# Optimization experiments

Measured on AMD Instinct MI355X. Metric: run time of the kernel, lower is better.

The kernel has to match this reference:

```python
import jax, jax.numpy as jnp
import numpy as np

LN_EPS = 1e-5

def _layer_norm(x, gamma, beta):
    mu = x.mean(-1, keepdims=True)
    var = ((x - mu) ** 2).mean(-1, keepdims=True)
    return (x - mu) * jax.lax.rsqrt(var + LN_EPS) * gamma + beta

def _neg_sq_dist(q, p):
    # q: [B,Qtot,H], p: [B,N,H] -> [B,Qtot,N]
    return -jnp.sum((q[:, :, None, :] - p[:, None, :, :]) ** 2, axis=-1)

def setup_inputs() -> dict:
    key = jax.random.key(0)
    k1, k2 = jax.random.split(key)
    B, N, K, Q, H = 512, 10, 5, 5, 256
    Qtot = N * Q  # na_rate = 0
    return {
        "support": jax.random.normal(k1, (B, N * K, H), dtype=jnp.float32),
        "query": jax.random.normal(k2, (B, Qtot, H), dtype=jnp.float32),
        "ln_gamma": jnp.ones((H,), dtype=jnp.float32),
        "ln_beta": jnp.zeros((H,), dtype=jnp.float32),
        "N": N,
        "K": K,
        "Q": Q,
    }

def reference(support, query, ln_gamma, ln_beta, N, K, Q):
    B, _, H = support.shape
    s = _layer_norm(support, ln_gamma, ln_beta).reshape(B, N, K, H)
    q = _layer_norm(query, ln_gamma, ln_beta)          # [B, Qtot, H]
    Qtot = q.shape[1]

    M = s.mean(axis=2)                                  # [B, N, H] mean prototype
    # --- __rectify__ ---
    Xq = _neg_sq_dist(q, M)                             # [B, Qtot, N]
    Cq = jnp.argmax(Xq, axis=-1)                        # [B, Qtot] nearest proto
    # padded support memory [B, N, K+Qtot, H]
    Xp = jnp.pad(s, ((0, 0), (0, 0), (0, Qtot), (0, 0)))
    b_idx = jnp.arange(B)[:, None]
    q_idx = jnp.arange(Qtot)[None, :]
    # each (b,q) writes a unique slot q+K -> no collisions
    Xp = Xp.at[b_idx, Cq, q_idx + K].set(q)
    counts = jax.nn.one_hot(Cq, N, dtype=jnp.float32).sum(axis=1)  # [B, N]
    Xp_size = (K + counts)[:, :, None]                  # [B, N, 1]

    scores = jnp.einsum("bnsh,bnh->bns", Xp, M)[..., None]  # [B,N,S,1]
    M_cos = jax.nn.softmax(scores, axis=1)              # softmax over N dim
    proto = (M_cos * Xp).sum(axis=-2) / Xp_size          # [B, N, H]
    # --- logits ---
    logits = _neg_sq_dist(q, proto)                     # [B, Qtot, N]
    minn = logits.min(axis=-1, keepdims=True)
    logits = jnp.concatenate([logits, minn - 1.0], axis=-1)  # [B, Qtot, N+1]
    pred = jnp.argmax(logits.reshape(-1, N + 1), axis=1)
    return logits, pred
```

## Files before the change

kernel.cpp:

```cpp
#include <hip/hip_runtime.h>
#include <math.h>

#define LN_EPS 1e-5f

constexpr int Nn  = 10;
constexpr int Kk  = 5;
constexpr int Hh  = 256;
constexpr int QT  = 50;
constexpr int NP1 = 11;

template<int CTRL, int RM>
__device__ __forceinline__ float dpp_term(float x) {
    return __int_as_float(__builtin_amdgcn_update_dpp(
        0, __float_as_int(x), CTRL, RM, 0xf, true));
}

__device__ __forceinline__ float sum16_bcast(float v) {
    v += dpp_term<0xB1,  0xf>(v);
    v += dpp_term<0x4E,  0xf>(v);
    v += dpp_term<0x124, 0xf>(v);
    v += dpp_term<0x128, 0xf>(v);
    return v;
}
__device__ __forceinline__ float sum64_lane63(float v) {
    v += dpp_term<0x111, 0xf>(v);
    v += dpp_term<0x112, 0xf>(v);
    v += dpp_term<0x114, 0xf>(v);
    v += dpp_term<0x118, 0xf>(v);
    v += dpp_term<0x142, 0xa>(v);
    v += dpp_term<0x143, 0xc>(v);
    return v;
}
__device__ __forceinline__ float rdlane(float v, int l) {
    return __int_as_float(__builtin_amdgcn_readlane(__float_as_int(v), l));
}
__device__ __forceinline__ float wave64_sum_bcast(float v) {
    return rdlane(sum64_lane63(v), 63);
}

__global__ __launch_bounds__(1024, 8) void proto_rectify_fused(
    const float* __restrict__ support, const float* __restrict__ query,
    const float* __restrict__ gamma,   const float* __restrict__ beta,
    float* __restrict__ out, int B)
{
    const int b    = blockIdx.x;
    const int tid  = threadIdx.x;
    const int lane = tid & 63;
    const int wave = tid >> 6;
    const int grp  = tid >> 4;
    const int sub  = tid & 15;

    __shared__ float g_s[Hh], bt_s[Hh];
    __shared__ float M_s[Nn][Hh];
    __shared__ float proto_s[Nn][Hh];
    __shared__ float nM_s[Nn], np_s[Nn];
    __shared__ float ny_s[QT];
    __shared__ float score_s[Nn * Kk];
    __shared__ float wsup_s[Nn * Kk];
    __shared__ float wq_s[QT];
    __shared__ int   cq_s[QT];
    __shared__ float sstat_s[Nn * Kk][2];
    __shared__ float qstat_s[QT][2];
    __shared__ int   cnt_s[Nn];

    const float* supB = support + (size_t)b * (Nn * Kk * Hh);
    const float* qryB = query   + (size_t)b * (QT * Hh);

    if (tid < Hh)          g_s[tid]       = gamma[tid];
    else if (tid < 2 * Hh) bt_s[tid - Hh] = beta[tid - Hh];
    if (tid < Nn)          cnt_s[tid]     = 0;

    if (wave < Nn) {
        const int n = wave;
        const float4 g4 = *reinterpret_cast<const float4*>(gamma + lane * 4);
        const float4 b4 = *reinterpret_cast<const float4*>(beta  + lane * 4);
        const float* rows = supB + (size_t)n * Kk * Hh;

        float y[Kk][4];
#pragma unroll
        for (int k = 0; k < Kk; ++k) {
            const float4 x = *reinterpret_cast<const float4*>(rows + k * Hh + lane * 4);
            float s  = x.x + x.y + x.z + x.w;
            float ss = x.x * x.x + x.y * x.y + x.z * x.z + x.w * x.w;
            s  = wave64_sum_bcast(s);
            ss = wave64_sum_bcast(ss);
            const float mu   = s * (1.0f / (float)Hh);
            const float rstd = rsqrtf(ss * (1.0f / (float)Hh) - mu * mu + LN_EPS);
            if (lane == 0) { sstat_s[n * Kk + k][0] = mu; sstat_s[n * Kk + k][1] = rstd; }
            y[k][0] = (x.x - mu) * rstd * g4.x + b4.x;
            y[k][1] = (x.y - mu) * rstd * g4.y + b4.y;
            y[k][2] = (x.z - mu) * rstd * g4.z + b4.z;
            y[k][3] = (x.w - mu) * rstd * g4.w + b4.w;
        }
        float Mv[4];
#pragma unroll
        for (int i = 0; i < 4; ++i)
            Mv[i] = (y[0][i] + y[1][i] + y[2][i] + y[3][i] + y[4][i]) / 5.0f;
        *reinterpret_cast<float4*>(&M_s[n][lane * 4]) =
            make_float4(Mv[0], Mv[1], Mv[2], Mv[3]);

        float pm = Mv[0] * Mv[0];
        pm = fmaf(Mv[1], Mv[1], pm); pm = fmaf(Mv[2], Mv[2], pm); pm = fmaf(Mv[3], Mv[3], pm);
        pm = sum64_lane63(pm);
        if (lane == 63) nM_s[n] = pm;

#pragma unroll
        for (int k = 0; k < Kk; ++k) {
            float p = y[k][0] * Mv[0];
            p = fmaf(y[k][1], Mv[1], p); p = fmaf(y[k][2], Mv[2], p); p = fmaf(y[k][3], Mv[3], p);
            p = sum64_lane63(p);
            if (lane == 63) score_s[n * Kk + k] = p;
        }
    }
    __syncthreads();

    if (grp < QT) {
        const int q = grp;
        const float* row = qryB + (size_t)q * Hh;
        float y16[16];
        float s = 0.f, ss = 0.f;
#pragma unroll
        for (int c = 0; c < 4; ++c) {
            const float4 x = *reinterpret_cast<const float4*>(row + c * 64 + sub * 4);
            y16[c * 4 + 0] = x.x; y16[c * 4 + 1] = x.y;
            y16[c * 4 + 2] = x.z; y16[c * 4 + 3] = x.w;
            s  += x.x + x.y + x.z + x.w;
            ss  = fmaf(x.x, x.x, ss); ss = fmaf(x.y, x.y, ss);
            ss  = fmaf(x.z, x.z, ss); ss = fmaf(x.w, x.w, ss);
        }
        s  = sum16_bcast(s);
        ss = sum16_bcast(ss);
        const float mu   = s * (1.0f / (float)Hh);
        const float rstd = rsqrtf(ss * (1.0f / (float)Hh) - mu * mu + LN_EPS);
        if (sub == 0) { qstat_s[q][0] = mu; qstat_s[q][1] = rstd; }

#pragma unroll
        for (int c = 0; c < 4; ++c) {
            const int h = c * 64 + sub * 4;
            const float4 gg = *reinterpret_cast<const float4*>(g_s + h);
            const float4 bb = *reinterpret_cast<const float4*>(bt_s + h);
            y16[c * 4 + 0] = (y16[c * 4 + 0] - mu) * rstd * gg.x + bb.x;
            y16[c * 4 + 1] = (y16[c * 4 + 1] - mu) * rstd * gg.y + bb.y;
            y16[c * 4 + 2] = (y16[c * 4 + 2] - mu) * rstd * gg.z + bb.z;
            y16[c * 4 + 3] = (y16[c * 4 + 3] - mu) * rstd * gg.w + bb.w;
        }
        float ny = 0.f;
#pragma unroll
        for (int j = 0; j < 16; ++j) ny = fmaf(y16[j], y16[j], ny);
        ny = sum16_bcast(ny);
        if (sub == 0) ny_s[q] = ny;

        float bestd = INFINITY, bestdot = 0.f;
        int bestn = 0;
#pragma unroll
        for (int n = 0; n < Nn; ++n) {
            float p = 0.f;
#pragma unroll
            for (int c = 0; c < 4; ++c) {
                const float4 mv = *reinterpret_cast<const float4*>(&M_s[n][c * 64 + sub * 4]);
                p = fmaf(y16[c * 4 + 0], mv.x, p);
                p = fmaf(y16[c * 4 + 1], mv.y, p);
                p = fmaf(y16[c * 4 + 2], mv.z, p);
                p = fmaf(y16[c * 4 + 3], mv.w, p);
            }
            p = sum16_bcast(p);
            const float d = nM_s[n] - 2.0f * p;
            if (d < bestd) { bestd = d; bestn = n; bestdot = p; }
        }
        if (sub == 0) {
            const float sc  = bestdot;
            const float mx  = fmaxf(sc, 0.f);
            const float e   = expf(sc - mx);
            const float den = e + (float)(Nn - 1) * expf(-mx);
            wq_s[q] = e / den;
            cq_s[q] = bestn;
            atomicAdd(&cnt_s[bestn], 1);
        }
    } else if (grp >= 56 && grp < 56 + Kk && sub == 0) {
        const int k = grp - 56;
        float mx = -INFINITY;
#pragma unroll
        for (int n = 0; n < Nn; ++n) mx = fmaxf(mx, score_s[n * Kk + k]);
        float e[Nn]; float den = 0.f;
#pragma unroll
        for (int n = 0; n < Nn; ++n) { e[n] = expf(score_s[n * Kk + k] - mx); den += e[n]; }
#pragma unroll
        for (int n = 0; n < Nn; ++n) wsup_s[n * Kk + k] = e[n] / den;
    }
    __syncthreads();

    if (wave < Nn) {
        const int n = wave;
        const float4 g4 = *reinterpret_cast<const float4*>(g_s  + lane * 4);
        const float4 b4 = *reinterpret_cast<const float4*>(bt_s + lane * 4);
        const float* rows = supB + (size_t)n * Kk * Hh;

        float acc[4] = {0.f, 0.f, 0.f, 0.f};
#pragma unroll
        for (int k = 0; k < Kk; ++k) {
            const float w    = wsup_s[n * Kk + k];
            const float mu   = sstat_s[n * Kk + k][0];
            const float rstd = sstat_s[n * Kk + k][1];
            const float4 x = *reinterpret_cast<const float4*>(rows + k * Hh + lane * 4);
            acc[0] = fmaf(w, (x.x - mu) * rstd * g4.x + b4.x, acc[0]);
            acc[1] = fmaf(w, (x.y - mu) * rstd * g4.y + b4.y, acc[1]);
            acc[2] = fmaf(w, (x.z - mu) * rstd * g4.z + b4.z, acc[2]);
            acc[3] = fmaf(w, (x.w - mu) * rstd * g4.w + b4.w, acc[3]);
        }
        int myc = -1; float myw = 0.f, mymu = 0.f, myr = 0.f;
        if (lane < QT) {
            myc  = cq_s[lane]; myw = wq_s[lane];
            mymu = qstat_s[lane][0]; myr = qstat_s[lane][1];
        }
        unsigned long long mask = __ballot(lane < QT && myc == n);
        while (mask) {
            const int q = __ffsll(mask) - 1;
            mask &= mask - 1;
            const float w    = rdlane(myw,  q);
            const float mu   = rdlane(mymu, q);
            const float rstd = rdlane(myr,  q);
            const float4 x = *reinterpret_cast<const float4*>(qryB + (size_t)q * Hh + lane * 4);
            acc[0] = fmaf(w, (x.x - mu) * rstd * g4.x + b4.x, acc[0]);
            acc[1] = fmaf(w, (x.y - mu) * rstd * g4.y + b4.y, acc[1]);
            acc[2] = fmaf(w, (x.z - mu) * rstd * g4.z + b4.z, acc[2]);
            acc[3] = fmaf(w, (x.w - mu) * rstd * g4.w + b4.w, acc[3]);
        }
        const float inv = 1.0f / (float)(Kk + cnt_s[n]);
        float pv[4];
#pragma unroll
        for (int i = 0; i < 4; ++i) pv[i] = acc[i] * inv;
        *reinterpret_cast<float4*>(&proto_s[n][lane * 4]) =
            make_float4(pv[0], pv[1], pv[2], pv[3]);
        float pp = pv[0] * pv[0];
        pp = fmaf(pv[1], pv[1], pp); pp = fmaf(pv[2], pv[2], pp); pp = fmaf(pv[3], pv[3], pp);
        pp = sum64_lane63(pp);
        if (lane == 63) np_s[n] = pp;
    }
    __syncthreads();

    if (grp < QT) {
        const int q = grp;
        const float* row  = qryB + (size_t)q * Hh;
        const float  mu   = qstat_s[q][0];
        const float  rstd = qstat_s[q][1];
        float y16[16];
#pragma unroll
        for (int c = 0; c < 4; ++c) {
            const int h = c * 64 + sub * 4;
            const float4 x  = *reinterpret_cast<const float4*>(row + h);
            const float4 gg = *reinterpret_cast<const float4*>(g_s + h);
            const float4 bb = *reinterpret_cast<const float4*>(bt_s + h);
            y16[c * 4 + 0] = (x.x - mu) * rstd * gg.x + bb.x;
            y16[c * 4 + 1] = (x.y - mu) * rstd * gg.y + bb.y;
            y16[c * 4 + 2] = (x.z - mu) * rstd * gg.z + bb.z;
            y16[c * 4 + 3] = (x.w - mu) * rstd * gg.w + bb.w;
        }
        const float ny = ny_s[q];

        float mine = 0.f, maxd = -INFINITY, bestd = INFINITY;
        int bestn = 0;
#pragma unroll
        for (int n = 0; n < Nn; ++n) {
            float p = 0.f;
#pragma unroll
            for (int c = 0; c < 4; ++c) {
                const float4 pv = *reinterpret_cast<const float4*>(&proto_s[n][c * 64 + sub * 4]);
                p = fmaf(y16[c * 4 + 0], pv.x, p);
                p = fmaf(y16[c * 4 + 1], pv.y, p);
                p = fmaf(y16[c * 4 + 2], pv.z, p);
                p = fmaf(y16[c * 4 + 3], pv.w, p);
            }
            p = sum16_bcast(p);
            const float d = ny + np_s[n] - 2.0f * p;
            if (sub == n) mine = d;
            maxd = fmaxf(maxd, d);
            if (d < bestd) { bestd = d; bestn = n; }
        }
        float* o = out + ((size_t)b * QT + q) * NP1;
        if (sub < Nn)       o[sub] = -mine;
        else if (sub == Nn) o[Nn]  = -maxd - 1.0f;
        else if (sub == Nn + 1)
            out[(size_t)B * QT * NP1 + (size_t)b * QT + q] = (float)bestn;
    }
}

extern "C" void kernel_launch(void* const* d_in, const int* in_sizes, int n_in,
                              void* d_out, int out_size, void* d_ws, size_t ws_size,
                              hipStream_t stream) {
    const float* support = (const float*)d_in[0];
    const float* query   = (const float*)d_in[1];
    const float* gamma   = (const float*)d_in[2];
    const float* beta    = (const float*)d_in[3];
    float* out = (float*)d_out;

    const int B = in_sizes[0] / (Nn * Kk * Hh);
    proto_rectify_fused<<<B, 1024, 0, stream>>>(support, query, gamma, beta, out, B);
}
```

Before: 28.64 us.

## Remap query phases from 16-lane groups to full-wave rows with register-resident M reuse

The two query phases now give each query row to a full wave, 64 lanes by 4 features, with each wave handling up to 4 queries strided by 16. Reductions switch from 16-lane DPP butterflies to full-wave DPP plus readlane broadcasts. Each M/proto float4 read from LDS is now reused across the wave's 4 queries, and the norms come in by readlane instead of LDS reads. This spreads the query work over all 16 waves instead of 13 and cuts LDS traffic, but each query now needs more reduction steps.

```diff
diff --git a/kernel.cpp b/kernel.cpp
--- a/kernel.cpp
+++ b/kernel.cpp
@@ -13,14 +13,6 @@
 __device__ __forceinline__ float dpp_term(float x) {
     return __int_as_float(__builtin_amdgcn_update_dpp(
         0, __float_as_int(x), CTRL, RM, 0xf, true));
-}
-
-__device__ __forceinline__ float sum16_bcast(float v) {
-    v += dpp_term<0xB1,  0xf>(v);
-    v += dpp_term<0x4E,  0xf>(v);
-    v += dpp_term<0x124, 0xf>(v);
-    v += dpp_term<0x128, 0xf>(v);
-    return v;
 }
 __device__ __forceinline__ float sum64_lane63(float v) {
     v += dpp_term<0x111, 0xf>(v);
@@ -47,8 +39,6 @@
     const int tid  = threadIdx.x;
     const int lane = tid & 63;
     const int wave = tid >> 6;
-    const int grp  = tid >> 4;
-    const int sub  = tid & 15;
 
     __shared__ float g_s[Hh], bt_s[Hh];
     __shared__ float M_s[Nn][Hh];
@@ -114,78 +104,80 @@
     }
     __syncthreads();
 
-    if (grp < QT) {
-        const int q = grp;
-        const float* row = qryB + (size_t)q * Hh;
-        float y16[16];
-        float s = 0.f, ss = 0.f;
-#pragma unroll
-        for (int c = 0; c < 4; ++c) {
-            const float4 x = *reinterpret_cast<const float4*>(row + c * 64 + sub * 4);
-            y16[c * 4 + 0] = x.x; y16[c * 4 + 1] = x.y;
-            y16[c * 4 + 2] = x.z; y16[c * 4 + 3] = x.w;
-            s  += x.x + x.y + x.z + x.w;
-            ss  = fmaf(x.x, x.x, ss); ss = fmaf(x.y, x.y, ss);
-            ss  = fmaf(x.z, x.z, ss); ss = fmaf(x.w, x.w, ss);
-        }
-        s  = sum16_bcast(s);
-        ss = sum16_bcast(ss);
-        const float mu   = s * (1.0f / (float)Hh);
-        const float rstd = rsqrtf(ss * (1.0f / (float)Hh) - mu * mu + LN_EPS);
-        if (sub == 0) { qstat_s[q][0] = mu; qstat_s[q][1] = rstd; }
-
-#pragma unroll
-        for (int c = 0; c < 4; ++c) {
-            const int h = c * 64 + sub * 4;
-            const float4 gg = *reinterpret_cast<const float4*>(g_s + h);
-            const float4 bb = *reinterpret_cast<const float4*>(bt_s + h);
-            y16[c * 4 + 0] = (y16[c * 4 + 0] - mu) * rstd * gg.x + bb.x;
-            y16[c * 4 + 1] = (y16[c * 4 + 1] - mu) * rstd * gg.y + bb.y;
-            y16[c * 4 + 2] = (y16[c * 4 + 2] - mu) * rstd * gg.z + bb.z;
-            y16[c * 4 + 3] = (y16[c * 4 + 3] - mu) * rstd * gg.w + bb.w;
-        }
-        float ny = 0.f;
-#pragma unroll
-        for (int j = 0; j < 16; ++j) ny = fmaf(y16[j], y16[j], ny);
-        ny = sum16_bcast(ny);
-        if (sub == 0) ny_s[q] = ny;
-
-        float bestd = INFINITY, bestdot = 0.f;
-        int bestn = 0;
+    {
+        const float4 g4 = *reinterpret_cast<const float4*>(g_s  + lane * 4);
+        const float4 b4 = *reinterpret_cast<const float4*>(bt_s + lane * 4);
+        const float nmv = (lane < Nn) ? nM_s[lane] : 0.f;
+
+        float4 ya[4];
+#pragma unroll
+        for (int i = 0; i < 4; ++i) {
+            const int q = i * 16 + wave;
+            if (q < QT) {
+                const float4 x = *reinterpret_cast<const float4*>(
+                    qryB + (size_t)q * Hh + lane * 4);
+                float s  = x.x + x.y + x.z + x.w;
+                float ss = fmaf(x.x, x.x, fmaf(x.y, x.y, fmaf(x.z, x.z, x.w * x.w)));
+                s  = wave64_sum_bcast(s);
+                ss = wave64_sum_bcast(ss);
+                const float mu   = s * (1.0f / (float)Hh);
+                const float rstd = rsqrtf(ss * (1.0f / (float)Hh) - mu * mu + LN_EPS);
+                ya[i].x = (x.x - mu) * rstd * g4.x + b4.x;
+                ya[i].y = (x.y - mu) * rstd * g4.y + b4.y;
+                ya[i].z = (x.z - mu) * rstd * g4.z + b4.z;
+                ya[i].w = (x.w - mu) * rstd * g4.w + b4.w;
+                float ny = fmaf(ya[i].x, ya[i].x, fmaf(ya[i].y, ya[i].y,
+                           fmaf(ya[i].z, ya[i].z, ya[i].w * ya[i].w)));
+                ny = sum64_lane63(ny);
+                if (lane == 63) ny_s[q] = ny;
+                if (lane == 0)  { qstat_s[q][0] = mu; qstat_s[q][1] = rstd; }
+            }
+        }
+
+        float bestd[4], bestdot[4]; int bestn[4];
+#pragma unroll
+        for (int i = 0; i < 4; ++i) { bestd[i] = INFINITY; bestdot[i] = 0.f; bestn[i] = 0; }
+
 #pragma unroll
         for (int n = 0; n < Nn; ++n) {
-            float p = 0.f;
-#pragma unroll
-            for (int c = 0; c < 4; ++c) {
-                const float4 mv = *reinterpret_cast<const float4*>(&M_s[n][c * 64 + sub * 4]);
-                p = fmaf(y16[c * 4 + 0], mv.x, p);
-                p = fmaf(y16[c * 4 + 1], mv.y, p);
-                p = fmaf(y16[c * 4 + 2], mv.z, p);
-                p = fmaf(y16[c * 4 + 3], mv.w, p);
-            }
-            p = sum16_bcast(p);
-            const float d = nM_s[n] - 2.0f * p;
-            if (d < bestd) { bestd = d; bestn = n; bestdot = p; }
-        }
-        if (sub == 0) {
-            const float sc  = bestdot;
-            const float mx  = fmaxf(sc, 0.f);
-            const float e   = expf(sc - mx);
-            const float den = e + (float)(Nn - 1) * expf(-mx);
-            wq_s[q] = e / den;
-            cq_s[q] = bestn;
-            atomicAdd(&cnt_s[bestn], 1);
-        }
-    } else if (grp >= 56 && grp < 56 + Kk && sub == 0) {
-        const int k = grp - 56;
-        float mx = -INFINITY;
-#pragma unroll
-        for (int n = 0; n < Nn; ++n) mx = fmaxf(mx, score_s[n * Kk + k]);
-        float e[Nn]; float den = 0.f;
-#pragma unroll
-        for (int n = 0; n < Nn; ++n) { e[n] = expf(score_s[n * Kk + k] - mx); den += e[n]; }
-#pragma unroll
-        for (int n = 0; n < Nn; ++n) wsup_s[n * Kk + k] = e[n] / den;
+            const float4 mv = *reinterpret_cast<const float4*>(&M_s[n][lane * 4]);
+            const float  nm = rdlane(nmv, n);
+#pragma unroll
+            for (int i = 0; i < 4; ++i) {
+                const int q = i * 16 + wave;
+                if (q < QT) {
+                    float p = fmaf(ya[i].x, mv.x, fmaf(ya[i].y, mv.y,
+                              fmaf(ya[i].z, mv.z, ya[i].w * mv.w)));
+                    p = wave64_sum_bcast(p);
+                    const float d = nm - 2.0f * p;
+                    if (d < bestd[i]) { bestd[i] = d; bestn[i] = n; bestdot[i] = p; }
+                }
+            }
+        }
+#pragma unroll
+        for (int i = 0; i < 4; ++i) {
+            const int q = i * 16 + wave;
+            if (q < QT && lane == 0) {
+                const float sc  = bestdot[i];
+                const float mx  = fmaxf(sc, 0.f);
+                const float e   = expf(sc - mx);
+                const float den = e + (float)(Nn - 1) * expf(-mx);
+                wq_s[q] = e / den;
+                cq_s[q] = bestn[i];
+                atomicAdd(&cnt_s[bestn[i]], 1);
+            }
+        }
+        if (wave == 15 && lane < Kk) {
+            const int k = lane;
+            float mx = -INFINITY;
+#pragma unroll
+            for (int n = 0; n < Nn; ++n) mx = fmaxf(mx, score_s[n * Kk + k]);
+            float e[Nn]; float den = 0.f;
+#pragma unroll
+            for (int n = 0; n < Nn; ++n) { e[n] = expf(score_s[n * Kk + k] - mx); den += e[n]; }
+#pragma unroll
+            for (int n = 0; n < Nn; ++n) wsup_s[n * Kk + k] = e[n] / den;
+        }
     }
     __syncthreads();
 
@@ -238,49 +230,60 @@
     }
     __syncthreads();
 
-    if (grp < QT) {
-        const int q = grp;
-        const float* row  = qryB + (size_t)q * Hh;
-        const float  mu   = qstat_s[q][0];
-        const float  rstd = qstat_s[q][1];
-        float y16[16];
-#pragma unroll
-        for (int c = 0; c < 4; ++c) {
-            const int h = c * 64 + sub * 4;
-            const float4 x  = *reinterpret_cast<const float4*>(row + h);
-            const float4 gg = *reinterpret_cast<const float4*>(g_s + h);
-            const float4 bb = *reinterpret_cast<const float4*>(bt_s + h);
-            y16[c * 4 + 0] = (x.x - mu) * rstd * gg.x + bb.x;
-            y16[c * 4 + 1] = (x.y - mu) * rstd * gg.y + bb.y;
-            y16[c * 4 + 2] = (x.z - mu) * rstd * gg.z + bb.z;
-            y16[c * 4 + 3] = (x.w - mu) * rstd * gg.w + bb.w;
-        }
-        const float ny = ny_s[q];
-
-        float mine = 0.f, maxd = -INFINITY, bestd = INFINITY;
-        int bestn = 0;
+    {
+        const float4 g4 = *reinterpret_cast<const float4*>(g_s  + lane * 4);
+        const float4 b4 = *reinterpret_cast<const float4*>(bt_s + lane * 4);
+        const float npv = (lane < Nn) ? np_s[lane] : 0.f;
+
+        float4 ya[4]; float nyq[4];
+#pragma unroll
+        for (int i = 0; i < 4; ++i) {
+            const int q = i * 16 + wave;
+            if (q < QT) {
+                const float mu   = qstat_s[q][0];
+                const float rstd = qstat_s[q][1];
+                const float4 x = *reinterpret_cast<const float4*>(
+                    qryB + (size_t)q * Hh + lane * 4);
+                ya[i].x = (x.x - mu) * rstd * g4.x + b4.x;
+                ya[i].y = (x.y - mu) * rstd * g4.y + b4.y;
+                ya[i].z = (x.z - mu) * rstd * g4.z + b4.z;
+                ya[i].w = (x.w - mu) * rstd * g4.w + b4.w;
+                nyq[i] = ny_s[q];
+            }
+        }
+        float ov[4], maxd[4], bestd[4]; int bestn[4];
+#pragma unroll
+        for (int i = 0; i < 4; ++i) { ov[i] = 0.f; maxd[i] = -INFINITY;
+                                      bestd[i] = INFINITY; bestn[i] = 0; }
 #pragma unroll
         for (int n = 0; n < Nn; ++n) {
-            float p = 0.f;
-#pragma unroll
-            for (int c = 0; c < 4; ++c) {
-                const float4 pv = *reinterpret_cast<const float4*>(&proto_s[n][c * 64 + sub * 4]);
-                p = fmaf(y16[c * 4 + 0], pv.x, p);
-                p = fmaf(y16[c * 4 + 1], pv.y, p);
-                p = fmaf(y16[c * 4 + 2], pv.z, p);
-                p = fmaf(y16[c * 4 + 3], pv.w, p);
-            }
-            p = sum16_bcast(p);
-            const float d = ny + np_s[n] - 2.0f * p;
-            if (sub == n) mine = d;
-            maxd = fmaxf(maxd, d);
-            if (d < bestd) { bestd = d; bestn = n; }
-        }
-        float* o = out + ((size_t)b * QT + q) * NP1;
-        if (sub < Nn)       o[sub] = -mine;
-        else if (sub == Nn) o[Nn]  = -maxd - 1.0f;
-        else if (sub == Nn + 1)
-            out[(size_t)B * QT * NP1 + (size_t)b * QT + q] = (float)bestn;
+            const float4 pv = *reinterpret_cast<const float4*>(&proto_s[n][lane * 4]);
+            const float  np = rdlane(npv, n);
+#pragma unroll
+            for (int i = 0; i < 4; ++i) {
+                const int q = i * 16 + wave;
+                if (q < QT) {
+                    float p = fmaf(ya[i].x, pv.x, fmaf(ya[i].y, pv.y,
+                              fmaf(ya[i].z, pv.z, ya[i].w * pv.w)));
+                    p = wave64_sum_bcast(p);
+                    const float d = nyq[i] + np - 2.0f * p;
+                    if (lane == n) ov[i] = d;
+                    maxd[i] = fmaxf(maxd[i], d);
+                    if (d < bestd[i]) { bestd[i] = d; bestn[i] = n; }
+                }
+            }
+        }
+#pragma unroll
+        for (int i = 0; i < 4; ++i) {
+            const int q = i * 16 + wave;
+            if (q < QT) {
+                if (lane == Nn) ov[i] = maxd[i] + 1.0f;
+                float* o = out + ((size_t)b * QT + q) * NP1;
+                if (lane <= Nn) o[lane] = -ov[i];
+                if (lane == Nn + 1)
+                    out[(size_t)B * QT * NP1 + (size_t)b * QT + q] = (float)bestn[i];
+            }
+        }
     }
 }
 
```

Result: slower. 45.04 us (+57.3%).

## Halve block size to 512 threads with strided loops over classes and queries

Applied to the files above, without the earlier changes.

Launches 512-thread blocks instead of 1024. Each wave now loops over classes with stride 8, and each 16-lane group handles up to two queries. The support softmax weights are recomputed per wave in registers and broadcast with readlane, replacing a separate phase and shared array. The prototype norms and squared norms are read through readlane instead of from shared memory. The goal is to cut idle threads (the old blocks left several waves unused) and raise block occupancy per CU, at the cost of serialising some work within waves.

```diff
diff --git a/kernel.cpp b/kernel.cpp
--- a/kernel.cpp
+++ b/kernel.cpp
@@ -14,7 +14,6 @@
     return __int_as_float(__builtin_amdgcn_update_dpp(
         0, __float_as_int(x), CTRL, RM, 0xf, true));
 }
-
 __device__ __forceinline__ float sum16_bcast(float v) {
     v += dpp_term<0xB1,  0xf>(v);
     v += dpp_term<0x4E,  0xf>(v);
@@ -38,7 +37,7 @@
     return rdlane(sum64_lane63(v), 63);
 }
 
-__global__ __launch_bounds__(1024, 8) void proto_rectify_fused(
+__global__ __launch_bounds__(512, 8) void proto_rectify_fused(
     const float* __restrict__ support, const float* __restrict__ query,
     const float* __restrict__ gamma,   const float* __restrict__ beta,
     float* __restrict__ out, int B)
@@ -56,7 +55,6 @@
     __shared__ float nM_s[Nn], np_s[Nn];
     __shared__ float ny_s[QT];
     __shared__ float score_s[Nn * Kk];
-    __shared__ float wsup_s[Nn * Kk];
     __shared__ float wq_s[QT];
     __shared__ int   cq_s[QT];
     __shared__ float sstat_s[Nn * Kk][2];
@@ -66,221 +64,237 @@
     const float* supB = support + (size_t)b * (Nn * Kk * Hh);
     const float* qryB = query   + (size_t)b * (QT * Hh);
 
-    if (tid < Hh)          g_s[tid]       = gamma[tid];
-    else if (tid < 2 * Hh) bt_s[tid - Hh] = beta[tid - Hh];
-    if (tid < Nn)          cnt_s[tid]     = 0;
-
-    if (wave < Nn) {
-        const int n = wave;
+    if (tid < Hh) g_s[tid] = gamma[tid];
+    else          bt_s[tid - Hh] = beta[tid - Hh];
+    if (tid < Nn) cnt_s[tid] = 0;
+
+    {
         const float4 g4 = *reinterpret_cast<const float4*>(gamma + lane * 4);
         const float4 b4 = *reinterpret_cast<const float4*>(beta  + lane * 4);
-        const float* rows = supB + (size_t)n * Kk * Hh;
-
-        float y[Kk][4];
-#pragma unroll
-        for (int k = 0; k < Kk; ++k) {
-            const float4 x = *reinterpret_cast<const float4*>(rows + k * Hh + lane * 4);
-            float s  = x.x + x.y + x.z + x.w;
-            float ss = x.x * x.x + x.y * x.y + x.z * x.z + x.w * x.w;
-            s  = wave64_sum_bcast(s);
-            ss = wave64_sum_bcast(ss);
-            const float mu   = s * (1.0f / (float)Hh);
-            const float rstd = rsqrtf(ss * (1.0f / (float)Hh) - mu * mu + LN_EPS);
-            if (lane == 0) { sstat_s[n * Kk + k][0] = mu; sstat_s[n * Kk + k][1] = rstd; }
-            y[k][0] = (x.x - mu) * rstd * g4.x + b4.x;
-            y[k][1] = (x.y - mu) * rstd * g4.y + b4.y;
-            y[k][2] = (x.z - mu) * rstd * g4.z + b4.z;
-            y[k][3] = (x.w - mu) * rstd * g4.w + b4.w;
-        }
-        float Mv[4];
-#pragma unroll
-        for (int i = 0; i < 4; ++i)
-            Mv[i] = (y[0][i] + y[1][i] + y[2][i] + y[3][i] + y[4][i]) / 5.0f;
-        *reinterpret_cast<float4*>(&M_s[n][lane * 4]) =
-            make_float4(Mv[0], Mv[1], Mv[2], Mv[3]);
-
-        float pm = Mv[0] * Mv[0];
-        pm = fmaf(Mv[1], Mv[1], pm); pm = fmaf(Mv[2], Mv[2], pm); pm = fmaf(Mv[3], Mv[3], pm);
-        pm = sum64_lane63(pm);
-        if (lane == 63) nM_s[n] = pm;
-
-#pragma unroll
-        for (int k = 0; k < Kk; ++k) {
-            float p = y[k][0] * Mv[0];
-            p = fmaf(y[k][1], Mv[1], p); p = fmaf(y[k][2], Mv[2], p); p = fmaf(y[k][3], Mv[3], p);
-            p = sum64_lane63(p);
-            if (lane == 63) score_s[n * Kk + k] = p;
+        for (int n = wave; n < Nn; n += 8) {
+            const float* rows = supB + (size_t)n * Kk * Hh;
+            float y[Kk][4];
+#pragma unroll
+            for (int k = 0; k < Kk; ++k) {
+                const float4 x = *reinterpret_cast<const float4*>(rows + k * Hh + lane * 4);
+                float s  = x.x + x.y + x.z + x.w;
+                float ss = x.x * x.x + x.y * x.y + x.z * x.z + x.w * x.w;
+                s  = wave64_sum_bcast(s);
+                ss = wave64_sum_bcast(ss);
+                const float mu   = s * (1.0f / (float)Hh);
+                const float rstd = rsqrtf(ss * (1.0f / (float)Hh) - mu * mu + LN_EPS);
+                if (lane == 0) { sstat_s[n * Kk + k][0] = mu; sstat_s[n * Kk + k][1] = rstd; }
+                y[k][0] = (x.x - mu) * rstd * g4.x + b4.x;
+                y[k][1] = (x.y - mu) * rstd * g4.y + b4.y;
+                y[k][2] = (x.z - mu) * rstd * g4.z + b4.z;
+                y[k][3] = (x.w - mu) * rstd * g4.w + b4.w;
+            }
+            float Mv[4];
+#pragma unroll
+            for (int i = 0; i < 4; ++i)
+                Mv[i] = (y[0][i] + y[1][i] + y[2][i] + y[3][i] + y[4][i]) / 5.0f;
+            *reinterpret_cast<float4*>(&M_s[n][lane * 4]) =
+                make_float4(Mv[0], Mv[1], Mv[2], Mv[3]);
+
+            float pm = Mv[0] * Mv[0];
+            pm = fmaf(Mv[1], Mv[1], pm); pm = fmaf(Mv[2], Mv[2], pm); pm = fmaf(Mv[3], Mv[3], pm);
+            pm = sum64_lane63(pm);
+            if (lane == 63) nM_s[n] = pm;
+
+#pragma unroll
+            for (int k = 0; k < Kk; ++k) {
+                float p = y[k][0] * Mv[0];
+                p = fmaf(y[k][1], Mv[1], p); p = fmaf(y[k][2], Mv[2], p); p = fmaf(y[k][3], Mv[3], p);
+                p = sum64_lane63(p);
+                if (lane == 63) score_s[n * Kk + k] = p;
+            }
         }
     }
     __syncthreads();
 
-    if (grp < QT) {
-        const int q = grp;
-        const float* row = qryB + (size_t)q * Hh;
-        float y16[16];
-        float s = 0.f, ss = 0.f;
-#pragma unroll
-        for (int c = 0; c < 4; ++c) {
-            const float4 x = *reinterpret_cast<const float4*>(row + c * 64 + sub * 4);
-            y16[c * 4 + 0] = x.x; y16[c * 4 + 1] = x.y;
-            y16[c * 4 + 2] = x.z; y16[c * 4 + 3] = x.w;
-            s  += x.x + x.y + x.z + x.w;
-            ss  = fmaf(x.x, x.x, ss); ss = fmaf(x.y, x.y, ss);
-            ss  = fmaf(x.z, x.z, ss); ss = fmaf(x.w, x.w, ss);
-        }
-        s  = sum16_bcast(s);
-        ss = sum16_bcast(ss);
-        const float mu   = s * (1.0f / (float)Hh);
-        const float rstd = rsqrtf(ss * (1.0f / (float)Hh) - mu * mu + LN_EPS);
-        if (sub == 0) { qstat_s[q][0] = mu; qstat_s[q][1] = rstd; }
-
-#pragma unroll
-        for (int c = 0; c < 4; ++c) {
-            const int h = c * 64 + sub * 4;
-            const float4 gg = *reinterpret_cast<const float4*>(g_s + h);
-            const float4 bb = *reinterpret_cast<const float4*>(bt_s + h);
-            y16[c * 4 + 0] = (y16[c * 4 + 0] - mu) * rstd * gg.x + bb.x;
-            y16[c * 4 + 1] = (y16[c * 4 + 1] - mu) * rstd * gg.y + bb.y;
-            y16[c * 4 + 2] = (y16[c * 4 + 2] - mu) * rstd * gg.z + bb.z;
-            y16[c * 4 + 3] = (y16[c * 4 + 3] - mu) * rstd * gg.w + bb.w;
-        }
-        float ny = 0.f;
-#pragma unroll
-        for (int j = 0; j < 16; ++j) ny = fmaf(y16[j], y16[j], ny);
-        ny = sum16_bcast(ny);
-        if (sub == 0) ny_s[q] = ny;
-
-        float bestd = INFINITY, bestdot = 0.f;
-        int bestn = 0;
-#pragma unroll
-        for (int n = 0; n < Nn; ++n) {
-            float p = 0.f;
-#pragma unroll
-            for (int c = 0; c < 4; ++c) {
-                const float4 mv = *reinterpret_cast<const float4*>(&M_s[n][c * 64 + sub * 4]);
-                p = fmaf(y16[c * 4 + 0], mv.x, p);
-                p = fmaf(y16[c * 4 + 1], mv.y, p);
-                p = fmaf(y16[c * 4 + 2], mv.z, p);
-                p = fmaf(y16[c * 4 + 3], mv.w, p);
-            }
-            p = sum16_bcast(p);
-            const float d = nM_s[n] - 2.0f * p;
-            if (d < bestd) { bestd = d; bestn = n; bestdot = p; }
-        }
-        if (sub == 0) {
-            const float sc  = bestdot;
-            const float mx  = fmaxf(sc, 0.f);
-            const float e   = expf(sc - mx);
-            const float den = e + (float)(Nn - 1) * expf(-mx);
-            wq_s[q] = e / den;
-            cq_s[q] = bestn;
-            atomicAdd(&cnt_s[bestn], 1);
-        }
-    } else if (grp >= 56 && grp < 56 + Kk && sub == 0) {
-        const int k = grp - 56;
-        float mx = -INFINITY;
-#pragma unroll
-        for (int n = 0; n < Nn; ++n) mx = fmaxf(mx, score_s[n * Kk + k]);
-        float e[Nn]; float den = 0.f;
-#pragma unroll
-        for (int n = 0; n < Nn; ++n) { e[n] = expf(score_s[n * Kk + k] - mx); den += e[n]; }
-#pragma unroll
-        for (int n = 0; n < Nn; ++n) wsup_s[n * Kk + k] = e[n] / den;
+    {
+        const float nmv = (lane < Nn) ? nM_s[lane] : 0.f;
+#pragma unroll
+        for (int it = 0; it < 2; ++it) {
+            const int q = grp + it * 32;
+            if (q < QT) {
+                const float* row = qryB + (size_t)q * Hh;
+                float y16[16];
+                float s = 0.f, ss = 0.f;
+#pragma unroll
+                for (int c = 0; c < 4; ++c) {
+                    const float4 x = *reinterpret_cast<const float4*>(row + c * 64 + sub * 4);
+                    y16[c * 4 + 0] = x.x; y16[c * 4 + 1] = x.y;
+                    y16[c * 4 + 2] = x.z; y16[c * 4 + 3] = x.w;
+                    s  += x.x + x.y + x.z + x.w;
+                    ss  = fmaf(x.x, x.x, ss); ss = fmaf(x.y, x.y, ss);
+                    ss  = fmaf(x.z, x.z, ss); ss = fmaf(x.w, x.w, ss);
+                }
+                s  = sum16_bcast(s);
+                ss = sum16_bcast(ss);
+                const float mu   = s * (1.0f / (float)Hh);
+                const float rstd = rsqrtf(ss * (1.0f / (float)Hh) - mu * mu + LN_EPS);
+                if (sub == 0) { qstat_s[q][0] = mu; qstat_s[q][1] = rstd; }
+
+#pragma unroll
+                for (int c = 0; c < 4; ++c) {
+                    const int h = c * 64 + sub * 4;
+                    const float4 gg = *reinterpret_cast<const float4*>(g_s + h);
+                    const float4 bb = *reinterpret_cast<const float4*>(bt_s + h);
+                    y16[c * 4 + 0] = (y16[c * 4 + 0] - mu) * rstd * gg.x + bb.x;
+                    y16[c * 4 + 1] = (y16[c * 4 + 1] - mu) * rstd * gg.y + bb.y;
+                    y16[c * 4 + 2] = (y16[c * 4 + 2] - mu) * rstd * gg.z + bb.z;
+                    y16[c * 4 + 3] = (y16[c * 4 + 3] - mu) * rstd * gg.w + bb.w;
+                }
+                float ny = 0.f;
+#pragma unroll
+                for (int j = 0; j < 16; ++j) ny = fmaf(y16[j], y16[j], ny);
+                ny = sum16_bcast(ny);
+                if (sub == 0) ny_s[q] = ny;
+
+                float bestd = INFINITY, bestdot = 0.f;
+                int bestn = 0;
+#pragma unroll
+                for (int n = 0; n < Nn; ++n) {
+                    float p = 0.f;
+#pragma unroll
+                    for (int c = 0; c < 4; ++c) {
+                        const float4 mv = *reinterpret_cast<const float4*>(&M_s[n][c * 64 + sub * 4]);
+                        p = fmaf(y16[c * 4 + 0], mv.x, p);
+                        p = fmaf(y16[c * 4 + 1], mv.y, p);
+                        p = fmaf(y16[c * 4 + 2], mv.z, p);
+                        p = fmaf(y16[c * 4 + 3], mv.w, p);
+                    }
+                    p = sum16_bcast(p);
+                    const float d = rdlane(nmv, n) - 2.0f * p;
+                    if (d < bestd) { bestd = d; bestn = n; bestdot = p; }
+                }
+                if (sub == 0) {
+                    const float sc  = bestdot;
+                    const float mx  = fmaxf(sc, 0.f);
+                    const float e   = expf(sc - mx);
+                    const float den = e + (float)(Nn - 1) * expf(-mx);
+                    wq_s[q] = e / den;
+                    cq_s[q] = bestn;
+                    atomicAdd(&cnt_s[bestn], 1);
+                }
+            }
+        }
     }
     __syncthreads();
 
-    if (wave < Nn) {
-        const int n = wave;
+    {
         const float4 g4 = *reinterpret_cast<const float4*>(g_s  + lane * 4);
         const float4 b4 = *reinterpret_cast<const float4*>(bt_s + lane * 4);
-        const float* rows = supB + (size_t)n * Kk * Hh;
-
-        float acc[4] = {0.f, 0.f, 0.f, 0.f};
-#pragma unroll
-        for (int k = 0; k < Kk; ++k) {
-            const float w    = wsup_s[n * Kk + k];
-            const float mu   = sstat_s[n * Kk + k][0];
-            const float rstd = sstat_s[n * Kk + k][1];
-            const float4 x = *reinterpret_cast<const float4*>(rows + k * Hh + lane * 4);
-            acc[0] = fmaf(w, (x.x - mu) * rstd * g4.x + b4.x, acc[0]);
-            acc[1] = fmaf(w, (x.y - mu) * rstd * g4.y + b4.y, acc[1]);
-            acc[2] = fmaf(w, (x.z - mu) * rstd * g4.z + b4.z, acc[2]);
-            acc[3] = fmaf(w, (x.w - mu) * rstd * g4.w + b4.w, acc[3]);
-        }
         int myc = -1; float myw = 0.f, mymu = 0.f, myr = 0.f;
         if (lane < QT) {
             myc  = cq_s[lane]; myw = wq_s[lane];
             mymu = qstat_s[lane][0]; myr = qstat_s[lane][1];
         }
-        unsigned long long mask = __ballot(lane < QT && myc == n);
-        while (mask) {
-            const int q = __ffsll(mask) - 1;
-            mask &= mask - 1;
-            const float w    = rdlane(myw,  q);
-            const float mu   = rdlane(mymu, q);
-            const float rstd = rdlane(myr,  q);
-            const float4 x = *reinterpret_cast<const float4*>(qryB + (size_t)q * Hh + lane * 4);
-            acc[0] = fmaf(w, (x.x - mu) * rstd * g4.x + b4.x, acc[0]);
-            acc[1] = fmaf(w, (x.y - mu) * rstd * g4.y + b4.y, acc[1]);
-            acc[2] = fmaf(w, (x.z - mu) * rstd * g4.z + b4.z, acc[2]);
-            acc[3] = fmaf(w, (x.w - mu) * rstd * g4.w + b4.w, acc[3]);
-        }
-        const float inv = 1.0f / (float)(Kk + cnt_s[n]);
-        float pv[4];
-#pragma unroll
-        for (int i = 0; i < 4; ++i) pv[i] = acc[i] * inv;
-        *reinterpret_cast<float4*>(&proto_s[n][lane * 4]) =
-            make_float4(pv[0], pv[1], pv[2], pv[3]);
-        float pp = pv[0] * pv[0];
-        pp = fmaf(pv[1], pv[1], pp); pp = fmaf(pv[2], pv[2], pp); pp = fmaf(pv[3], pv[3], pp);
-        pp = sum64_lane63(pp);
-        if (lane == 63) np_s[n] = pp;
+        for (int n = wave; n < Nn; n += 8) {
+            float wown = 0.f;
+            if (lane < Kk) {
+                float mx = -INFINITY;
+#pragma unroll
+                for (int nn = 0; nn < Nn; ++nn) mx = fmaxf(mx, score_s[nn * Kk + lane]);
+                float den = 0.f, mye = 0.f;
+#pragma unroll
+                for (int nn = 0; nn < Nn; ++nn) {
+                    const float e = expf(score_s[nn * Kk + lane] - mx);
+                    den += e;
+                    if (nn == n) mye = e;
+                }
+                wown = mye / den;
+            }
+            const float* rows = supB + (size_t)n * Kk * Hh;
+            float acc[4] = {0.f, 0.f, 0.f, 0.f};
+#pragma unroll
+            for (int k = 0; k < Kk; ++k) {
+                const float w    = rdlane(wown, k);
+                const float mu   = sstat_s[n * Kk + k][0];
+                const float rstd = sstat_s[n * Kk + k][1];
+                const float4 x = *reinterpret_cast<const float4*>(rows + k * Hh + lane * 4);
+                acc[0] = fmaf(w, (x.x - mu) * rstd * g4.x + b4.x, acc[0]);
+                acc[1] = fmaf(w, (x.y - mu) * rstd * g4.y + b4.y, acc[1]);
+                acc[2] = fmaf(w, (x.z - mu) * rstd * g4.z + b4.z, acc[2]);
+                acc[3] = fmaf(w, (x.w - mu) * rstd * g4.w + b4.w, acc[3]);
+            }
+            unsigned long long mask = __ballot(lane < QT && myc == n);
+            while (mask) {
+                const int q = __ffsll(mask) - 1;
+                mask &= mask - 1;
+                const float w    = rdlane(myw,  q);
+                const float mu   = rdlane(mymu, q);
+                const float rstd = rdlane(myr,  q);
+                const float4 x = *reinterpret_cast<const float4*>(qryB + (size_t)q * Hh + lane * 4);
+                acc[0] = fmaf(w, (x.x - mu) * rstd * g4.x + b4.x, acc[0]);
+                acc[1] = fmaf(w, (x.y - mu) * rstd * g4.y + b4.y, acc[1]);
+                acc[2] = fmaf(w, (x.z - mu) * rstd * g4.z + b4.z, acc[2]);
+                acc[3] = fmaf(w, (x.w - mu) * rstd * g4.w + b4.w, acc[3]);
+            }
+            const float inv = 1.0f / (float)(Kk + cnt_s[n]);
+            float pv[4];
+#pragma unroll
+            for (int i = 0; i < 4; ++i) pv[i] = acc[i] * inv;
+            *reinterpret_cast<float4*>(&proto_s[n][lane * 4]) =
+                make_float4(pv[0], pv[1], pv[2], pv[3]);
+            float pp = pv[0] * pv[0];
+            pp = fmaf(pv[1], pv[1], pp); pp = fmaf(pv[2], pv[2], pp); pp = fmaf(pv[3], pv[3], pp);
+            pp = sum64_lane63(pp);
+            if (lane == 63) np_s[n] = pp;
+        }
     }
     __syncthreads();
 
-    if (grp < QT) {
-        const int q = grp;
-        const float* row  = qryB + (size_t)q * Hh;
-        const float  mu   = qstat_s[q][0];
-        const float  rstd = qstat_s[q][1];
-        float y16[16];
-#pragma unroll
-        for (int c = 0; c < 4; ++c) {
-            const int h = c * 64 + sub * 4;
-            const float4 x  = *reinterpret_cast<const float4*>(row + h);
-            const float4 gg = *reinterpret_cast<const float4*>(g_s + h);
-            const float4 bb = *reinterpret_cast<const float4*>(bt_s + h);
-            y16[c * 4 + 0] = (x.x - mu) * rstd * gg.x + bb.x;
-            y16[c * 4 + 1] = (x.y - mu) * rstd * gg.y + bb.y;
-            y16[c * 4 + 2] = (x.z - mu) * rstd * gg.z + bb.z;
-            y16[c * 4 + 3] = (x.w - mu) * rstd * gg.w + bb.w;
-        }
-        const float ny = ny_s[q];
-
-        float mine = 0.f, maxd = -INFINITY, bestd = INFINITY;
-        int bestn = 0;
-#pragma unroll
-        for (int n = 0; n < Nn; ++n) {
-            float p = 0.f;
-#pragma unroll
-            for (int c = 0; c < 4; ++c) {
-                const float4 pv = *reinterpret_cast<const float4*>(&proto_s[n][c * 64 + sub * 4]);
-                p = fmaf(y16[c * 4 + 0], pv.x, p);
-                p = fmaf(y16[c * 4 + 1], pv.y, p);
-                p = fmaf(y16[c * 4 + 2], pv.z, p);
-                p = fmaf(y16[c * 4 + 3], pv.w, p);
-            }
-            p = sum16_bcast(p);
-            const float d = ny + np_s[n] - 2.0f * p;
-            if (sub == n) mine = d;
-            maxd = fmaxf(maxd, d);
-            if (d < bestd) { bestd = d; bestn = n; }
-        }
-        float* o = out + ((size_t)b * QT + q) * NP1;
-        if (sub < Nn)       o[sub] = -mine;
-        else if (sub == Nn) o[Nn]  = -maxd - 1.0f;
-        else if (sub == Nn + 1)
-            out[(size_t)B * QT * NP1 + (size_t)b * QT + q] = (float)bestn;
+    {
+        const float npv = (lane < Nn) ? np_s[lane] : 0.f;
+#pragma unroll
+        for (int it = 0; it < 2; ++it) {
+            const int q = grp + it * 32;
+            if (q < QT) {
+                const float* row  = qryB + (size_t)q * Hh;
+                const float  mu   = qstat_s[q][0];
+                const float  rstd = qstat_s[q][1];
+                float y16[16];
+#pragma unroll
+                for (int c = 0; c < 4; ++c) {
+                    const int h = c * 64 + sub * 4;
+                    const float4 x  = *reinterpret_cast<const float4*>(row + h);
+                    const float4 gg = *reinterpret_cast<const float4*>(g_s + h);
+                    const float4 bb = *reinterpret_cast<const float4*>(bt_s + h);
+                    y16[c * 4 + 0] = (x.x - mu) * rstd * gg.x + bb.x;
+                    y16[c * 4 + 1] = (x.y - mu) * rstd * gg.y + bb.y;
+                    y16[c * 4 + 2] = (x.z - mu) * rstd * gg.z + bb.z;
+                    y16[c * 4 + 3] = (x.w - mu) * rstd * gg.w + bb.w;
+                }
+                const float ny = ny_s[q];
+
+                float ov = 0.f, maxd = -INFINITY, bestd = INFINITY;
+                int bestn = 0;
+#pragma unroll
+                for (int n = 0; n < Nn; ++n) {
+                    float p = 0.f;
+#pragma unroll
+                    for (int c = 0; c < 4; ++c) {
+                        const float4 pv = *reinterpret_cast<const float4*>(&proto_s[n][c * 64 + sub * 4]);
+                        p = fmaf(y16[c * 4 + 0], pv.x, p);
+                        p = fmaf(y16[c * 4 + 1], pv.y, p);
+                        p = fmaf(y16[c * 4 + 2], pv.z, p);
+                        p = fmaf(y16[c * 4 + 3], pv.w, p);
+                    }
+                    p = sum16_bcast(p);
+                    const float d = ny + rdlane(npv, n) - 2.0f * p;
+                    if (sub == n) ov = d;
+                    maxd = fmaxf(maxd, d);
+                    if (d < bestd) { bestd = d; bestn = n; }
+                }
+                if (sub == Nn) ov = maxd + 1.0f;
+                float* o = out + ((size_t)b * QT + q) * NP1;
+                if (sub <= Nn) o[sub] = -ov;
+                if (sub == Nn + 1)
+                    out[(size_t)B * QT * NP1 + (size_t)b * QT + q] = (float)bestn;
+            }
+        }
     }
 }
 
@@ -294,5 +308,5 @@
     float* out = (float*)d_out;
 
     const int B = in_sizes[0] / (Nn * Kk * Hh);
-    proto_rectify_fused<<<B, 1024, 0, stream>>>(support, query, gamma, beta, out, B);
-}
+    proto_rectify_fused<<<B, 512, 0, stream>>>(support, query, gamma, beta, out, B);
+}
```

After: 33.02 us. 15.3% more time.
